# Performance work log

Measured on AMD Instinct MI355X. Metric: run time of the kernel, lower is better.

## Reference

```python
import jax, jax.numpy as jnp
import numpy as np

N_NODES = 100_000
N_EDGES = 1_600_000  # avg degree 16
D_FEAT = 64


def setup_inputs() -> dict:
    key = jax.random.key(0)
    k_x, k_val, k_src, k_dst = jax.random.split(key, 4)
    x = jax.random.normal(k_x, (N_NODES, D_FEAT), dtype=jnp.float32)
    edge_val = jax.random.uniform(k_val, (N_EDGES,), dtype=jnp.float32)
    edge_src = jax.random.randint(k_src, (N_EDGES,), 0, N_NODES, dtype=jnp.int32)
    edge_dst = jax.random.randint(k_dst, (N_EDGES,), 0, N_NODES, dtype=jnp.int32)
    return {"x": x, "edge_val": edge_val, "edge_src": edge_src, "edge_dst": edge_dst}


def reference(x, edge_val, edge_src, edge_dst):
    # out = adj @ x  with adj in COO form:
    # out[dst] += val * x[src]   (sparse-dense matmul, SpMM)
    msgs = x[edge_src] * edge_val[:, None]          # [E, D] gather + scale
    out = jax.ops.segment_sum(msgs, edge_dst, num_segments=N_NODES)  # [N, D] scatter-add
    return out
```

## Files before the change

### kernel.cpp

```cpp
#include <hip/hip_runtime.h>

#define N_NODES 100000
#define N_EDGES 1600000
#define D_FEAT 64
#define NPB 128
#define K_BUCKETS 782
#define CAP 2304
#define A_BLOCKS 400
#define A_CHUNK 4000
#define A_THREADS 512
#define S_THREADS 256

typedef long long i64;
typedef float f4 __attribute__((ext_vector_type(4)));

__global__ __launch_bounds__(A_THREADS) void scatterA(
        const int* __restrict__ src, const int* __restrict__ dst,
        const float* __restrict__ val, int* __restrict__ cursor,
        int2* __restrict__ bdata) {
    __shared__ int cnt[K_BUCKETS];
    __shared__ int lstart[K_BUCKETS];
    __shared__ int adj[K_BUCKETS];
    __shared__ int cur[K_BUCKETS];
    __shared__ int sums[A_THREADS];
    __shared__ int2 staged[A_CHUNK];
    __shared__ int gidx[A_CHUNK];
    const int t = threadIdx.x;
    const int base = blockIdx.x * A_CHUNK;

    for (int i = t; i < K_BUCKETS; i += A_THREADS) cnt[i] = 0;
    __syncthreads();
    for (int j = t; j < A_CHUNK; j += A_THREADS)
        atomicAdd(&cnt[dst[base + j] >> 7], 1);
    __syncthreads();

    int s0 = 0, s1 = 0;
    if (t < K_BUCKETS / 2) { s0 = cnt[2 * t]; s1 = cnt[2 * t + 1]; }
    sums[t] = s0 + s1;
    __syncthreads();
    for (int off = 1; off < A_THREADS; off <<= 1) {
        const int u = (t >= off) ? sums[t - off] : 0;
        __syncthreads();
        sums[t] += u;
        __syncthreads();
    }
    if (t < K_BUCKETS / 2) {
        const int excl = sums[t] - (s0 + s1);
        lstart[2 * t]     = excl;
        lstart[2 * t + 1] = excl + s0;
    }
    __syncthreads();

    for (int i = t; i < K_BUCKETS; i += A_THREADS) {
        const int c = cnt[i];
        const int ls = lstart[i];
        cur[i] = ls;
        adj[i] = c ? (i * CAP + atomicAdd(&cursor[i], c)) - ls : 0;
    }
    __syncthreads();

    for (int j = t; j < A_CHUNK; j += A_THREADS) {
        const int e = base + j;
        const int d = dst[e];
        const int b = d >> 7;
        const int s = __builtin_nontemporal_load(src + e);
        const float v = __builtin_nontemporal_load(val + e);
        const int r = atomicAdd(&cur[b], 1);
        staged[r] = make_int2(s | ((d & 127) << 17), __float_as_int(v));
        gidx[r] = adj[b] + r;
    }
    __syncthreads();

    for (int j = t; j < A_CHUNK; j += A_THREADS) {
        const int2 pv = staged[j];
        const i64 raw = (i64)(unsigned)pv.x | ((i64)pv.y << 32);
        __builtin_nontemporal_store(raw, (i64*)(bdata + gidx[j]));
    }
}

__global__ __launch_bounds__(S_THREADS) void sort_spmm(
        const float* __restrict__ x, const int2* __restrict__ bdata,
        const int* __restrict__ cursor, float* __restrict__ out) {
    __shared__ int2 sh_e[CAP];
    __shared__ int2 sh_s[CAP];
    __shared__ int cnt[NPB];
    __shared__ int cur[NPB];
    const int b = blockIdx.x;
    const int count = min(cursor[b], CAP);
    const int base = b * CAP;
    const int t = threadIdx.x;

    if (t < NPB) cnt[t] = 0;
    __syncthreads();
    for (int j = t; j < count; j += S_THREADS) {
        const i64 raw = __builtin_nontemporal_load((const i64*)(bdata + base + j));
        const int2 e = make_int2((int)(unsigned)raw, (int)(raw >> 32));
        sh_e[j] = e;
        atomicAdd(&cnt[e.x >> 17], 1);
    }
    __syncthreads();
    const int v = (t < NPB) ? cnt[t] : 0;
    for (int off = 1; off < NPB; off <<= 1) {
        int u = 0;
        if (t < NPB && t >= off) u = cnt[t - off];
        __syncthreads();
        if (t < NPB) cnt[t] += u;
        __syncthreads();
    }
    if (t < NPB) cur[t] = cnt[t] - v;
    __syncthreads();
    for (int j = t; j < count; j += S_THREADS) {
        const int2 pv = sh_e[j];
        const int dl = pv.x >> 17;
        const int slot = atomicAdd(&cur[dl], 1);
        sh_s[slot] = make_int2(pv.x & 0x1FFFF, pv.y);
    }
    __syncthreads();

    const int lane = t & 15;
    const int rg = t >> 4;
    const int row0 = b * NPB;
    for (int r = rg; r < NPB; r += S_THREADS / 16) {
        const int node = row0 + r;
        if (node >= N_NODES) continue;
        const int beg = r ? cnt[r - 1] : 0;
        const int end = cnt[r];
        float4 acc = {0.f, 0.f, 0.f, 0.f};
        int j = beg;
        for (; j + 4 <= end; j += 4) {
            const int2 p0 = sh_s[j];
            const int2 p1 = sh_s[j + 1];
            const int2 p2 = sh_s[j + 2];
            const int2 p3 = sh_s[j + 3];
            const float4 m0 = ((const float4*)(x + (size_t)p0.x * D_FEAT))[lane];
            const float4 m1 = ((const float4*)(x + (size_t)p1.x * D_FEAT))[lane];
            const float4 m2 = ((const float4*)(x + (size_t)p2.x * D_FEAT))[lane];
            const float4 m3 = ((const float4*)(x + (size_t)p3.x * D_FEAT))[lane];
            const float v0 = __int_as_float(p0.y);
            const float v1 = __int_as_float(p1.y);
            const float v2 = __int_as_float(p2.y);
            const float v3 = __int_as_float(p3.y);
            acc.x += v0 * m0.x + v1 * m1.x + v2 * m2.x + v3 * m3.x;
            acc.y += v0 * m0.y + v1 * m1.y + v2 * m2.y + v3 * m3.y;
            acc.z += v0 * m0.z + v1 * m1.z + v2 * m2.z + v3 * m3.z;
            acc.w += v0 * m0.w + v1 * m1.w + v2 * m2.w + v3 * m3.w;
        }
        for (; j < end; ++j) {
            const int2 p0 = sh_s[j];
            const float4 m0 = ((const float4*)(x + (size_t)p0.x * D_FEAT))[lane];
            const float v0 = __int_as_float(p0.y);
            acc.x += v0 * m0.x;
            acc.y += v0 * m0.y;
            acc.z += v0 * m0.z;
            acc.w += v0 * m0.w;
        }
        const f4 accv = {acc.x, acc.y, acc.z, acc.w};
        __builtin_nontemporal_store(accv, (f4*)(out + (size_t)node * D_FEAT) + lane);
    }
}

extern "C" void kernel_launch(void* const* d_in, const int* in_sizes, int n_in,
                              void* d_out, int out_size, void* d_ws, size_t ws_size,
                              hipStream_t stream) {
    const float* x        = (const float*)d_in[0];
    const float* edge_val = (const float*)d_in[1];
    const int*   edge_src = (const int*)d_in[2];
    const int*   edge_dst = (const int*)d_in[3];
    float* out = (float*)d_out;

    int* ws     = (int*)d_ws;
    int* cursor = ws;
    int2* bdata = (int2*)(ws + K_BUCKETS);

    hipMemsetAsync(cursor, 0, K_BUCKETS * sizeof(int), stream);

    scatterA <<<A_BLOCKS, A_THREADS, 0, stream>>>(edge_src, edge_dst, edge_val,
                                                  cursor, bdata);
    sort_spmm<<<K_BUCKETS, S_THREADS, 0, stream>>>(x, bdata, cursor, out);
}
```

Baseline: 171.1 us.

## Fuse memset, bucket scatter and sort-SpMM into one cooperative persistent kernel

Adds a single cooperative kernel that runs 782 blocks, each bucketing a chunk of about 2047 edges. Grid-wide syncs replace the separate memset and the two kernel launches, and a shared-memory union lets both phases reuse the same LDS. The aim is to remove launch gaps and the memset dispatch between stages. In exchange it pays two grid barriers, needs all 782 blocks to be co-resident (the host checks occupancy and falls back to the old path otherwise), and runs the scatter phase with more, smaller blocks.

```diff
diff --git a/kernel.cpp b/kernel.cpp
--- a/kernel.cpp
+++ b/kernel.cpp
@@ -1,4 +1,7 @@
 #include <hip/hip_runtime.h>
+#include <hip/hip_cooperative_groups.h>
+
+namespace cg = cooperative_groups;
 
 #define N_NODES 100000
 #define N_EDGES 1600000
@@ -6,13 +9,177 @@
 #define NPB 128
 #define K_BUCKETS 782
 #define CAP 2304
+#define CH 2047
+#define T 256
+
 #define A_BLOCKS 400
 #define A_CHUNK 4000
 #define A_THREADS 512
-#define S_THREADS 256
 
 typedef long long i64;
 typedef float f4 __attribute__((ext_vector_type(4)));
+
+union SharedU {
+    struct {
+        int cnt[K_BUCKETS];
+        int lstart[K_BUCKETS];
+        int adj[K_BUCKETS];
+        int cur[K_BUCKETS];
+        int sums[T];
+        int2 staged[CH];
+        int gidx[CH];
+    } p1;
+    struct {
+        int2 sh_e[CAP];
+        int2 sh_s[CAP];
+        int cnt[NPB];
+        int cur[NPB];
+    } p2;
+};
+
+__global__ __launch_bounds__(T, 4) void fused(
+        const float* __restrict__ x, const float* __restrict__ val,
+        const int* __restrict__ src, const int* __restrict__ dst,
+        int* __restrict__ cursor, int2* __restrict__ bdata,
+        float* __restrict__ out) {
+    __shared__ SharedU sh;
+    const int t = threadIdx.x;
+    const int blk = blockIdx.x;
+
+    if (blk == 0)
+        for (int i = t; i < K_BUCKETS; i += T) cursor[i] = 0;
+
+    const int e0 = blk * CH;
+    const int e1 = min(N_EDGES, e0 + CH);
+    const int n  = e1 - e0;
+    for (int i = t; i < K_BUCKETS; i += T) sh.p1.cnt[i] = 0;
+    __syncthreads();
+    for (int j = t; j < n; j += T)
+        atomicAdd(&sh.p1.cnt[dst[e0 + j] >> 7], 1);
+    __syncthreads();
+    int s[4];
+    int tot = 0;
+#pragma unroll
+    for (int k = 0; k < 4; ++k) {
+        const int i = t * 4 + k;
+        s[k] = (i < K_BUCKETS) ? sh.p1.cnt[i] : 0;
+        tot += s[k];
+    }
+    sh.p1.sums[t] = tot;
+    __syncthreads();
+    for (int off = 1; off < T; off <<= 1) {
+        const int u = (t >= off) ? sh.p1.sums[t - off] : 0;
+        __syncthreads();
+        sh.p1.sums[t] += u;
+        __syncthreads();
+    }
+    int run = sh.p1.sums[t] - tot;
+#pragma unroll
+    for (int k = 0; k < 4; ++k) {
+        const int i = t * 4 + k;
+        if (i < K_BUCKETS) sh.p1.lstart[i] = run;
+        run += s[k];
+    }
+    __syncthreads();
+
+    cg::this_grid().sync();
+
+    for (int i = t; i < K_BUCKETS; i += T) {
+        const int c = sh.p1.cnt[i];
+        const int ls = sh.p1.lstart[i];
+        sh.p1.cur[i] = ls;
+        sh.p1.adj[i] = c ? (i * CAP + atomicAdd(&cursor[i], c)) - ls : 0;
+    }
+    __syncthreads();
+    for (int j = t; j < n; j += T) {
+        const int e = e0 + j;
+        const int d = dst[e];
+        const int b = d >> 7;
+        const int sv = __builtin_nontemporal_load(src + e);
+        const float vv = __builtin_nontemporal_load(val + e);
+        const int r = atomicAdd(&sh.p1.cur[b], 1);
+        sh.p1.staged[r] = make_int2(sv | ((d & 127) << 17), __float_as_int(vv));
+        sh.p1.gidx[r] = sh.p1.adj[b] + r;
+    }
+    __syncthreads();
+    for (int j = t; j < n; j += T) {
+        const int2 pv = sh.p1.staged[j];
+        const i64 raw = (i64)(unsigned)pv.x | ((i64)pv.y << 32);
+        __builtin_nontemporal_store(raw, (i64*)(bdata + sh.p1.gidx[j]));
+    }
+
+    cg::this_grid().sync();
+
+    const int count = min(cursor[blk], CAP);
+    const int gbase = blk * CAP;
+    if (t < NPB) sh.p2.cnt[t] = 0;
+    __syncthreads();
+    for (int j = t; j < count; j += T) {
+        const i64 raw = __builtin_nontemporal_load((const i64*)(bdata + gbase + j));
+        const int2 e = make_int2((int)(unsigned)raw, (int)(raw >> 32));
+        sh.p2.sh_e[j] = e;
+        atomicAdd(&sh.p2.cnt[e.x >> 17], 1);
+    }
+    __syncthreads();
+    const int deg = (t < NPB) ? sh.p2.cnt[t] : 0;
+    for (int off = 1; off < NPB; off <<= 1) {
+        int u = 0;
+        if (t < NPB && t >= off) u = sh.p2.cnt[t - off];
+        __syncthreads();
+        if (t < NPB) sh.p2.cnt[t] += u;
+        __syncthreads();
+    }
+    if (t < NPB) sh.p2.cur[t] = sh.p2.cnt[t] - deg;
+    __syncthreads();
+    for (int j = t; j < count; j += T) {
+        const int2 pv = sh.p2.sh_e[j];
+        const int dl = pv.x >> 17;
+        const int slot = atomicAdd(&sh.p2.cur[dl], 1);
+        sh.p2.sh_s[slot] = make_int2(pv.x & 0x1FFFF, pv.y);
+    }
+    __syncthreads();
+
+    const int lane = t & 15;
+    const int rg = t >> 4;
+    const int row0 = blk * NPB;
+    for (int r = rg; r < NPB; r += T / 16) {
+        const int node = row0 + r;
+        if (node >= N_NODES) continue;
+        const int beg = r ? sh.p2.cnt[r - 1] : 0;
+        const int end = sh.p2.cnt[r];
+        float4 acc = {0.f, 0.f, 0.f, 0.f};
+        int j = beg;
+        for (; j + 4 <= end; j += 4) {
+            const int2 p0 = sh.p2.sh_s[j];
+            const int2 p1 = sh.p2.sh_s[j + 1];
+            const int2 p2 = sh.p2.sh_s[j + 2];
+            const int2 p3 = sh.p2.sh_s[j + 3];
+            const float4 m0 = ((const float4*)(x + (size_t)p0.x * D_FEAT))[lane];
+            const float4 m1 = ((const float4*)(x + (size_t)p1.x * D_FEAT))[lane];
+            const float4 m2 = ((const float4*)(x + (size_t)p2.x * D_FEAT))[lane];
+            const float4 m3 = ((const float4*)(x + (size_t)p3.x * D_FEAT))[lane];
+            const float v0 = __int_as_float(p0.y);
+            const float v1 = __int_as_float(p1.y);
+            const float v2 = __int_as_float(p2.y);
+            const float v3 = __int_as_float(p3.y);
+            acc.x += v0 * m0.x + v1 * m1.x + v2 * m2.x + v3 * m3.x;
+            acc.y += v0 * m0.y + v1 * m1.y + v2 * m2.y + v3 * m3.y;
+            acc.z += v0 * m0.z + v1 * m1.z + v2 * m2.z + v3 * m3.z;
+            acc.w += v0 * m0.w + v1 * m1.w + v2 * m2.w + v3 * m3.w;
+        }
+        for (; j < end; ++j) {
+            const int2 p0 = sh.p2.sh_s[j];
+            const float4 m0 = ((const float4*)(x + (size_t)p0.x * D_FEAT))[lane];
+            const float v0 = __int_as_float(p0.y);
+            acc.x += v0 * m0.x;
+            acc.y += v0 * m0.y;
+            acc.z += v0 * m0.z;
+            acc.w += v0 * m0.w;
+        }
+        const f4 accv = {acc.x, acc.y, acc.z, acc.w};
+        __builtin_nontemporal_store(accv, (f4*)(out + (size_t)node * D_FEAT) + lane);
+    }
+}
 
 __global__ __launch_bounds__(A_THREADS) void scatterA(
         const int* __restrict__ src, const int* __restrict__ dst,
@@ -33,7 +200,6 @@
     for (int j = t; j < A_CHUNK; j += A_THREADS)
         atomicAdd(&cnt[dst[base + j] >> 7], 1);
     __syncthreads();
-
     int s0 = 0, s1 = 0;
     if (t < K_BUCKETS / 2) { s0 = cnt[2 * t]; s1 = cnt[2 * t + 1]; }
     sums[t] = s0 + s1;
@@ -50,7 +216,6 @@
         lstart[2 * t + 1] = excl + s0;
     }
     __syncthreads();
-
     for (int i = t; i < K_BUCKETS; i += A_THREADS) {
         const int c = cnt[i];
         const int ls = lstart[i];
@@ -58,19 +223,17 @@
         adj[i] = c ? (i * CAP + atomicAdd(&cursor[i], c)) - ls : 0;
     }
     __syncthreads();
-
     for (int j = t; j < A_CHUNK; j += A_THREADS) {
         const int e = base + j;
         const int d = dst[e];
         const int b = d >> 7;
-        const int s = __builtin_nontemporal_load(src + e);
-        const float v = __builtin_nontemporal_load(val + e);
+        const int sv = __builtin_nontemporal_load(src + e);
+        const float vv = __builtin_nontemporal_load(val + e);
         const int r = atomicAdd(&cur[b], 1);
-        staged[r] = make_int2(s | ((d & 127) << 17), __float_as_int(v));
+        staged[r] = make_int2(sv | ((d & 127) << 17), __float_as_int(vv));
         gidx[r] = adj[b] + r;
     }
     __syncthreads();
-
     for (int j = t; j < A_CHUNK; j += A_THREADS) {
         const int2 pv = staged[j];
         const i64 raw = (i64)(unsigned)pv.x | ((i64)pv.y << 32);
@@ -78,7 +241,7 @@
     }
 }
 
-__global__ __launch_bounds__(S_THREADS) void sort_spmm(
+__global__ __launch_bounds__(T) void sort_spmm(
         const float* __restrict__ x, const int2* __restrict__ bdata,
         const int* __restrict__ cursor, float* __restrict__ out) {
     __shared__ int2 sh_e[CAP];
@@ -92,7 +255,7 @@
 
     if (t < NPB) cnt[t] = 0;
     __syncthreads();
-    for (int j = t; j < count; j += S_THREADS) {
+    for (int j = t; j < count; j += T) {
         const i64 raw = __builtin_nontemporal_load((const i64*)(bdata + base + j));
         const int2 e = make_int2((int)(unsigned)raw, (int)(raw >> 32));
         sh_e[j] = e;
@@ -109,7 +272,7 @@
     }
     if (t < NPB) cur[t] = cnt[t] - v;
     __syncthreads();
-    for (int j = t; j < count; j += S_THREADS) {
+    for (int j = t; j < count; j += T) {
         const int2 pv = sh_e[j];
         const int dl = pv.x >> 17;
         const int slot = atomicAdd(&cur[dl], 1);
@@ -120,7 +283,7 @@
     const int lane = t & 15;
     const int rg = t >> 4;
     const int row0 = b * NPB;
-    for (int r = rg; r < NPB; r += S_THREADS / 16) {
+    for (int r = rg; r < NPB; r += T / 16) {
         const int node = row0 + r;
         if (node >= N_NODES) continue;
         const int beg = r ? cnt[r - 1] : 0;
@@ -172,9 +335,33 @@
     int* cursor = ws;
     int2* bdata = (int2*)(ws + K_BUCKETS);
 
+    static int coop = -1;
+    if (coop < 0) {
+        int nb = 0;
+        hipDeviceProp_t prop;
+        int dev = 0;
+        int ncu = 256;
+        if (hipGetDevice(&dev) == hipSuccess &&
+            hipGetDeviceProperties(&prop, dev) == hipSuccess)
+            ncu = prop.multiProcessorCount;
+        if (hipOccupancyMaxActiveBlocksPerMultiprocessor(&nb, fused, T, 0) == hipSuccess)
+            coop = (nb * ncu >= K_BUCKETS) ? 1 : 0;
+        else
+            coop = 0;
+    }
+
+    if (coop == 1) {
+        void* args[] = {(void*)&x, (void*)&edge_val, (void*)&edge_src,
+                        (void*)&edge_dst, (void*)&cursor, (void*)&bdata,
+                        (void*)&out};
+        if (hipLaunchCooperativeKernel(fused, dim3(K_BUCKETS), dim3(T), args,
+                                       0, stream) == hipSuccess)
+            return;
+        coop = 0;
+    }
+
     hipMemsetAsync(cursor, 0, K_BUCKETS * sizeof(int), stream);
-
     scatterA <<<A_BLOCKS, A_THREADS, 0, stream>>>(edge_src, edge_dst, edge_val,
                                                   cursor, bdata);
-    sort_spmm<<<K_BUCKETS, S_THREADS, 0, stream>>>(x, bdata, cursor, out);
+    sort_spmm<<<K_BUCKETS, T, 0, stream>>>(x, bdata, cursor, out);
 }
```

After: 340.3 us. 98.9% more time.

## Halve nodes per bucket, unroll gather loop by 8, add occupancy launch bound

Applied to the files above, without the earlier changes.

Buckets now cover 64 nodes instead of 128, which doubles the bucket count and halves the per-bucket capacity. The partition kernel's scan is reworked so each thread handles four buckets, and the sort/SpMM kernel's shared-memory footprint shrinks, with a min-blocks hint of 6. The intent is more resident blocks and more memory-level parallelism in the gather. An 8-way unrolled inner loop adds more independent row loads in flight, at the cost of register pressure. Smaller CAP raises the risk of bucket overflow, which would silently drop edges.

```diff
diff --git a/kernel.cpp b/kernel.cpp
--- a/kernel.cpp
+++ b/kernel.cpp
@@ -3,9 +3,9 @@
 #define N_NODES 100000
 #define N_EDGES 1600000
 #define D_FEAT 64
-#define NPB 128
-#define K_BUCKETS 782
-#define CAP 2304
+#define NPB 64
+#define K_BUCKETS 1563
+#define CAP 1216
 #define A_BLOCKS 400
 #define A_CHUNK 4000
 #define A_THREADS 512
@@ -31,12 +31,18 @@
     for (int i = t; i < K_BUCKETS; i += A_THREADS) cnt[i] = 0;
     __syncthreads();
     for (int j = t; j < A_CHUNK; j += A_THREADS)
-        atomicAdd(&cnt[dst[base + j] >> 7], 1);
-    __syncthreads();
-
-    int s0 = 0, s1 = 0;
-    if (t < K_BUCKETS / 2) { s0 = cnt[2 * t]; s1 = cnt[2 * t + 1]; }
-    sums[t] = s0 + s1;
+        atomicAdd(&cnt[dst[base + j] >> 6], 1);
+    __syncthreads();
+
+    int s[4];
+    int tot = 0;
+#pragma unroll
+    for (int k = 0; k < 4; ++k) {
+        const int i = t * 4 + k;
+        s[k] = (i < K_BUCKETS) ? cnt[i] : 0;
+        tot += s[k];
+    }
+    sums[t] = tot;
     __syncthreads();
     for (int off = 1; off < A_THREADS; off <<= 1) {
         const int u = (t >= off) ? sums[t - off] : 0;
@@ -44,10 +50,12 @@
         sums[t] += u;
         __syncthreads();
     }
-    if (t < K_BUCKETS / 2) {
-        const int excl = sums[t] - (s0 + s1);
-        lstart[2 * t]     = excl;
-        lstart[2 * t + 1] = excl + s0;
+    int run = sums[t] - tot;
+#pragma unroll
+    for (int k = 0; k < 4; ++k) {
+        const int i = t * 4 + k;
+        if (i < K_BUCKETS) lstart[i] = run;
+        run += s[k];
     }
     __syncthreads();
 
@@ -62,11 +70,11 @@
     for (int j = t; j < A_CHUNK; j += A_THREADS) {
         const int e = base + j;
         const int d = dst[e];
-        const int b = d >> 7;
-        const int s = __builtin_nontemporal_load(src + e);
-        const float v = __builtin_nontemporal_load(val + e);
+        const int b = d >> 6;
+        const int sv = __builtin_nontemporal_load(src + e);
+        const float vv = __builtin_nontemporal_load(val + e);
         const int r = atomicAdd(&cur[b], 1);
-        staged[r] = make_int2(s | ((d & 127) << 17), __float_as_int(v));
+        staged[r] = make_int2(sv | ((d & 63) << 17), __float_as_int(vv));
         gidx[r] = adj[b] + r;
     }
     __syncthreads();
@@ -78,7 +86,7 @@
     }
 }
 
-__global__ __launch_bounds__(S_THREADS) void sort_spmm(
+__global__ __launch_bounds__(S_THREADS, 6) void sort_spmm(
         const float* __restrict__ x, const int2* __restrict__ bdata,
         const int* __restrict__ cursor, float* __restrict__ out) {
     __shared__ int2 sh_e[CAP];
@@ -99,7 +107,7 @@
         atomicAdd(&cnt[e.x >> 17], 1);
     }
     __syncthreads();
-    const int v = (t < NPB) ? cnt[t] : 0;
+    const int deg = (t < NPB) ? cnt[t] : 0;
     for (int off = 1; off < NPB; off <<= 1) {
         int u = 0;
         if (t < NPB && t >= off) u = cnt[t - off];
@@ -107,7 +115,7 @@
         if (t < NPB) cnt[t] += u;
         __syncthreads();
     }
-    if (t < NPB) cur[t] = cnt[t] - v;
+    if (t < NPB) cur[t] = cnt[t] - deg;
     __syncthreads();
     for (int j = t; j < count; j += S_THREADS) {
         const int2 pv = sh_e[j];
@@ -127,6 +135,40 @@
         const int end = cnt[r];
         float4 acc = {0.f, 0.f, 0.f, 0.f};
         int j = beg;
+        for (; j + 8 <= end; j += 8) {
+            const int2 pa0 = sh_s[j];
+            const int2 pa1 = sh_s[j + 1];
+            const int2 pa2 = sh_s[j + 2];
+            const int2 pa3 = sh_s[j + 3];
+            const int2 pb0 = sh_s[j + 4];
+            const int2 pb1 = sh_s[j + 5];
+            const int2 pb2 = sh_s[j + 6];
+            const int2 pb3 = sh_s[j + 7];
+            const float4 ma0 = ((const float4*)(x + (size_t)pa0.x * D_FEAT))[lane];
+            const float4 ma1 = ((const float4*)(x + (size_t)pa1.x * D_FEAT))[lane];
+            const float4 ma2 = ((const float4*)(x + (size_t)pa2.x * D_FEAT))[lane];
+            const float4 ma3 = ((const float4*)(x + (size_t)pa3.x * D_FEAT))[lane];
+            const float4 mb0 = ((const float4*)(x + (size_t)pb0.x * D_FEAT))[lane];
+            const float4 mb1 = ((const float4*)(x + (size_t)pb1.x * D_FEAT))[lane];
+            const float4 mb2 = ((const float4*)(x + (size_t)pb2.x * D_FEAT))[lane];
+            const float4 mb3 = ((const float4*)(x + (size_t)pb3.x * D_FEAT))[lane];
+            const float va0 = __int_as_float(pa0.y);
+            const float va1 = __int_as_float(pa1.y);
+            const float va2 = __int_as_float(pa2.y);
+            const float va3 = __int_as_float(pa3.y);
+            const float vb0 = __int_as_float(pb0.y);
+            const float vb1 = __int_as_float(pb1.y);
+            const float vb2 = __int_as_float(pb2.y);
+            const float vb3 = __int_as_float(pb3.y);
+            acc.x += va0 * ma0.x + va1 * ma1.x + va2 * ma2.x + va3 * ma3.x
+                   + vb0 * mb0.x + vb1 * mb1.x + vb2 * mb2.x + vb3 * mb3.x;
+            acc.y += va0 * ma0.y + va1 * ma1.y + va2 * ma2.y + va3 * ma3.y
+                   + vb0 * mb0.y + vb1 * mb1.y + vb2 * mb2.y + vb3 * mb3.y;
+            acc.z += va0 * ma0.z + va1 * ma1.z + va2 * ma2.z + va3 * ma3.z
+                   + vb0 * mb0.z + vb1 * mb1.z + vb2 * mb2.z + vb3 * mb3.z;
+            acc.w += va0 * ma0.w + va1 * ma1.w + va2 * ma2.w + va3 * ma3.w
+                   + vb0 * mb0.w + vb1 * mb1.w + vb2 * mb2.w + vb3 * mb3.w;
+        }
         for (; j + 4 <= end; j += 4) {
             const int2 p0 = sh_s[j];
             const int2 p1 = sh_s[j + 1];
@@ -170,7 +212,7 @@
 
     int* ws     = (int*)d_ws;
     int* cursor = ws;
-    int2* bdata = (int2*)(ws + K_BUCKETS);
+    int2* bdata = (int2*)(ws + ((K_BUCKETS + 1) & ~1));
 
     hipMemsetAsync(cursor, 0, K_BUCKETS * sizeof(int), stream);
 
```

New measurement: 181.9 us. 1.06x slower.
